# Optimization experiments

Measured on AMD Instinct MI355X. Metric: run time of the kernel, lower is better.

The kernel has to match this reference:

```python
import jax, jax.numpy as jnp
import numpy as np

NUM_EMBEDDINGS = 1024
EMBEDDING_DIM = 64
COMMITMENT_COST = 0.25


def setup_inputs() -> dict:
    key = jax.random.key(0)
    k_in, k_emb = jax.random.split(key)
    inputs = jax.random.normal(k_in, (256, 512, EMBEDDING_DIM), dtype=jnp.float32)
    # nn.init.uniform_(weight, -1/K, 1/K)
    bound = 1.0 / NUM_EMBEDDINGS
    embeddings = jax.random.uniform(
        k_emb, (NUM_EMBEDDINGS, EMBEDDING_DIM), dtype=jnp.float32,
        minval=-bound, maxval=bound)
    return {"inputs": inputs, "embeddings": embeddings}


def reference(inputs, embeddings):
    D = embeddings.shape[1]
    flat = inputs.reshape(-1, D)  # [N, D]
    distances = (
        jnp.sum(flat ** 2, axis=1, keepdims=True)
        - 2.0 * flat @ embeddings.T
        + jnp.sum(embeddings ** 2, axis=1)
    )
    encoding_indices = jnp.argmin(distances, axis=1)  # [N]
    quantized = embeddings[encoding_indices].reshape(inputs.shape)
    e_latent_loss = jnp.mean((jax.lax.stop_gradient(quantized) - inputs) ** 2)
    q_latent_loss = jnp.mean((quantized - jax.lax.stop_gradient(inputs)) ** 2)
    loss = q_latent_loss + COMMITMENT_COST * e_latent_loss
    # straight-through estimator
    quantized = inputs + jax.lax.stop_gradient(quantized - inputs)
    return quantized, loss
```

## Files before the change

### kernel.cpp

```cpp
#include <hip/hip_runtime.h>


typedef __attribute__((ext_vector_type(4))) float f32x4;
typedef __attribute__((ext_vector_type(2))) unsigned long long u64x2;

constexpr int N_ROWS = 256 * 512;
constexpr int D      = 64;
constexpr int K      = 1024;
constexpr int TPB    = 256;
constexpr int ROWS_PER_WAVE  = 16;
constexpr int ROWS_PER_BLOCK = 64;
constexpr int NBLK   = N_ROWS / ROWS_PER_BLOCK;
constexpr int CHUNK  = 128;
constexpr int NCHUNK = K / CHUNK;
constexpr int TPC    = CHUNK / 16;

__global__ __launch_bounds__(64) void vq_prep_kernel(
    const float* __restrict__ emb, uint4* __restrict__ ebf) {
  int k = blockIdx.x * 64 + threadIdx.x;
  if (k >= K) return;
  const float* e = emb + (size_t)k * D;
  const int crow = k & 15;
  uint4* row = ebf + ((size_t)(k >> 4) * 1024 + (size_t)crow * 64) / 16;
  const int sw = (crow >> 1) & 3;
#pragma unroll
  for (int s = 0; s < 4; ++s) {
    float4 a0 = *(const float4*)(e + s * 8);
    float4 a1 = *(const float4*)(e + s * 8 + 4);
    float4 b0 = *(const float4*)(e + 32 + s * 8);
    float4 b1 = *(const float4*)(e + 32 + s * 8 + 4);
    const float sc = -1024.f;
    int d0 = 0, d1 = 0, d2 = 0, d3 = 0;
    d0 = __builtin_amdgcn_cvt_pk_fp8_f32(sc * a0.x, sc * a0.y, d0, false);
    d0 = __builtin_amdgcn_cvt_pk_fp8_f32(sc * a0.z, sc * a0.w, d0, true);
    d1 = __builtin_amdgcn_cvt_pk_fp8_f32(sc * a1.x, sc * a1.y, d1, false);
    d1 = __builtin_amdgcn_cvt_pk_fp8_f32(sc * a1.z, sc * a1.w, d1, true);
    d2 = __builtin_amdgcn_cvt_pk_fp8_f32(sc * b0.x, sc * b0.y, d2, false);
    d2 = __builtin_amdgcn_cvt_pk_fp8_f32(sc * b0.z, sc * b0.w, d2, true);
    d3 = __builtin_amdgcn_cvt_pk_fp8_f32(sc * b1.x, sc * b1.y, d3, false);
    d3 = __builtin_amdgcn_cvt_pk_fp8_f32(sc * b1.z, sc * b1.w, d3, true);
    uint4 slot;
    slot.x = (unsigned)d0; slot.y = (unsigned)d1;
    slot.z = (unsigned)d2; slot.w = (unsigned)d3;
    row[s ^ sw] = slot;
  }
}

__global__ __launch_bounds__(TPB, 6) void vq_main_kernel(
    const float* __restrict__ x, const uint4* __restrict__ ebf,
    const float* __restrict__ emb, float* __restrict__ out,
    float* __restrict__ partial) {
  __shared__ uint4 se[2][CHUNK * 4];
  __shared__ int   s_bi[ROWS_PER_BLOCK];
  __shared__ float s_w[TPB / 64];

  const int tid  = threadIdx.x;
  const int wave = tid >> 6, lane = tid & 63;
  const int lrow = lane & 15;
  const int kseg = lane >> 4;

  uint4 st0[2];
#pragma unroll
  for (int i = 0; i < 2; ++i) st0[i] = ebf[i * 256 + tid];

  const size_t rbase =
      (size_t)blockIdx.x * ROWS_PER_BLOCK + (size_t)wave * ROWS_PER_WAVE;

  long long xa[2];
  {
    const float* p = x + (rbase + lrow) * D + kseg * 8;
#pragma unroll
    for (int h = 0; h < 2; ++h) {
      float4 a = *(const float4*)(p + h * 32);
      float4 b = *(const float4*)(p + h * 32 + 4);
      int d0 = 0, d1 = 0;
      d0 = __builtin_amdgcn_cvt_pk_fp8_f32(a.x, a.y, d0, false);
      d0 = __builtin_amdgcn_cvt_pk_fp8_f32(a.z, a.w, d0, true);
      d1 = __builtin_amdgcn_cvt_pk_fp8_f32(b.x, b.y, d1, false);
      d1 = __builtin_amdgcn_cvt_pk_fp8_f32(b.z, b.w, d1, true);
      xa[h] = (long long)(((unsigned long long)(unsigned)d1 << 32) |
                          (unsigned long long)(unsigned)d0);
    }
  }

#pragma unroll
  for (int i = 0; i < 2; ++i) se[0][i * 256 + tid] = st0[i];

  unsigned kmin[4];
#pragma unroll
  for (int j = 0; j < 4; ++j) kmin[j] = 0xFFFFFFFFu;

  const f32x4 c512 = {512.f, 512.f, 512.f, 512.f};

  __syncthreads();

  const int off = lrow * 64 + ((kseg ^ ((lrow >> 1) & 3)) << 4);

  int cur = 0;
  for (int c = 0; c < NCHUNK; ++c) {
    uint4 stg[2];
    if (c + 1 < NCHUNK) {
#pragma unroll
      for (int i = 0; i < 2; ++i)
        stg[i] = ebf[(c + 1) * 512 + i * 256 + tid];
    }

    const char* base = (const char*)&se[cur][0];
#pragma unroll
    for (int tt = 0; tt < TPC; ++tt) {
      u64x2 ev = *(const u64x2*)(base + (tt << 10) + off);
      const int kcode = c * CHUNK + tt * 16 + lrow;
      f32x4 acc = __builtin_amdgcn_mfma_f32_16x16x32_fp8_fp8(
          xa[0], (long long)ev[0], c512, 0, 0, 0);
      acc = __builtin_amdgcn_mfma_f32_16x16x32_fp8_fp8(
          xa[1], (long long)ev[1], acc, 0, 0, 0);
#pragma unroll
      for (int j = 0; j < 4; ++j) {
        unsigned key = (__builtin_bit_cast(unsigned, acc[j]) & 0xFFFFFC00u) |
                       (unsigned)kcode;
        kmin[j] = kmin[j] < key ? kmin[j] : key;
      }
    }

    if (c + 1 < NCHUNK) {
#pragma unroll
      for (int i = 0; i < 2; ++i) se[cur ^ 1][i * 256 + tid] = stg[i];
    }
    __syncthreads();
    cur ^= 1;
  }

#pragma unroll
  for (int m = 1; m <= 8; m <<= 1) {
#pragma unroll
    for (int j = 0; j < 4; ++j) {
      unsigned o = (unsigned)__shfl_xor((int)kmin[j], m, 64);
      kmin[j] = kmin[j] < o ? kmin[j] : o;
    }
  }

  if (lrow < 4) {
    unsigned v = (lrow == 0) ? kmin[0] : (lrow == 1) ? kmin[1]
               : (lrow == 2) ? kmin[2] : kmin[3];
    s_bi[wave * ROWS_PER_WAVE + kseg * 4 + lrow] = (int)(v & 1023u);
  }

  const int rig = lane >> 4;
  const int chk = lane & 15;
  float lp = 0.f;
#pragma unroll
  for (int g = 0; g < ROWS_PER_WAVE / 4; ++g) {
    const int wrow = g * 4 + rig;
    const size_t r = rbase + wrow;
    const int bi = s_bi[wave * ROWS_PER_WAVE + wrow];
    float4 xv = ((const float4*)(x + r * D))[chk];
    float4 qv = ((const float4*)(emb + (size_t)bi * D))[chk];
    float dx = qv.x - xv.x, dy = qv.y - xv.y;
    float dz = qv.z - xv.z, dw = qv.w - xv.w;
    lp = fmaf(dx, dx, lp); lp = fmaf(dy, dy, lp);
    lp = fmaf(dz, dz, lp); lp = fmaf(dw, dw, lp);
    float4 ov;
    ov.x = xv.x + dx; ov.y = xv.y + dy;
    ov.z = xv.z + dz; ov.w = xv.w + dw;
    ((float4*)(out + r * D))[chk] = ov;
  }

#pragma unroll
  for (int o2 = 32; o2 > 0; o2 >>= 1) lp += __shfl_down(lp, o2, 64);
  if (lane == 0) s_w[wave] = lp;
  __syncthreads();
  if (tid == 0)
    partial[blockIdx.x] = (s_w[0] + s_w[1]) + (s_w[2] + s_w[3]);
}

__global__ __launch_bounds__(256) void vq_loss_kernel(
    const float* __restrict__ partial, float* __restrict__ out) {
  __shared__ float wsum[4];
  int tid = threadIdx.x;
  float v = 0.f;
#pragma unroll
  for (int i = 0; i < NBLK / 256; ++i) v += partial[tid + i * 256];
#pragma unroll
  for (int off = 32; off > 0; off >>= 1) v += __shfl_down(v, off, 64);
  if ((tid & 63) == 0) wsum[tid >> 6] = v;
  __syncthreads();
  if (tid == 0) {
    float total = (wsum[0] + wsum[1]) + (wsum[2] + wsum[3]);
    out[(size_t)N_ROWS * D] = 1.25f * total / (float)((size_t)N_ROWS * D);
  }
}

extern "C" void kernel_launch(void* const* d_in, const int* in_sizes, int n_in,
                              void* d_out, int out_size, void* d_ws,
                              size_t ws_size, hipStream_t stream) {
  const float* x   = (const float*)d_in[0];
  const float* emb = (const float*)d_in[1];
  float* out = (float*)d_out;

  char* ws = (char*)d_ws;
  float* partial = (float*)ws;
  uint4* ebf     = (uint4*)(ws + 8192);

  vq_prep_kernel<<<16, 64, 0, stream>>>(emb, ebf);
  vq_main_kernel<<<NBLK, TPB, 0, stream>>>(x, ebf, emb, out, partial);
  vq_loss_kernel<<<1, 256, 0, stream>>>(partial, out);
}
```

Baseline: 34.46 us.

## Keep codebook quarters in registers per wave, drop LDS chunk pipeline

Each wave now holds a quarter of the fp8 codebook (256 codes) in registers and computes distances for all 64 block rows against it. This replaces the double-buffered LDS streaming of codebook chunks and its per-chunk barriers. Per-wave partial argmin keys are merged through a small shared array. The cost is much higher register pressure: each thread holds 16 uint4 of codebook data plus 16 kmin accumulators, and the occupancy hint drops from 6 to 3.

```diff
diff --git a/kernel.cpp b/kernel.cpp
--- a/kernel.cpp
+++ b/kernel.cpp
@@ -2,27 +2,22 @@
 
 
 typedef __attribute__((ext_vector_type(4))) float f32x4;
-typedef __attribute__((ext_vector_type(2))) unsigned long long u64x2;
 
 constexpr int N_ROWS = 256 * 512;
 constexpr int D      = 64;
 constexpr int K      = 1024;
 constexpr int TPB    = 256;
-constexpr int ROWS_PER_WAVE  = 16;
-constexpr int ROWS_PER_BLOCK = 64;
-constexpr int NBLK   = N_ROWS / ROWS_PER_BLOCK;
-constexpr int CHUNK  = 128;
-constexpr int NCHUNK = K / CHUNK;
-constexpr int TPC    = CHUNK / 16;
+constexpr int RPB    = 64;
+constexpr int NBLK   = N_ROWS / RPB;
+constexpr int KPW    = K / 4;
+constexpr int TPW    = KPW / 16;
 
 __global__ __launch_bounds__(64) void vq_prep_kernel(
     const float* __restrict__ emb, uint4* __restrict__ ebf) {
   int k = blockIdx.x * 64 + threadIdx.x;
   if (k >= K) return;
   const float* e = emb + (size_t)k * D;
-  const int crow = k & 15;
-  uint4* row = ebf + ((size_t)(k >> 4) * 1024 + (size_t)crow * 64) / 16;
-  const int sw = (crow >> 1) & 3;
+  uint4* row = ebf + (size_t)(k >> 4) * 64 + (size_t)(k & 15) * 4;
 #pragma unroll
   for (int s = 0; s < 4; ++s) {
     float4 a0 = *(const float4*)(e + s * 8);
@@ -42,33 +37,33 @@
     uint4 slot;
     slot.x = (unsigned)d0; slot.y = (unsigned)d1;
     slot.z = (unsigned)d2; slot.w = (unsigned)d3;
-    row[s ^ sw] = slot;
+    row[s] = slot;
   }
 }
 
-__global__ __launch_bounds__(TPB, 6) void vq_main_kernel(
+__global__ __launch_bounds__(TPB, 3) void vq_main_kernel(
     const float* __restrict__ x, const uint4* __restrict__ ebf,
     const float* __restrict__ emb, float* __restrict__ out,
     float* __restrict__ partial) {
-  __shared__ uint4 se[2][CHUNK * 4];
-  __shared__ int   s_bi[ROWS_PER_BLOCK];
-  __shared__ float s_w[TPB / 64];
+  __shared__ unsigned s_key[RPB][4];
+  __shared__ float    s_w[4];
 
   const int tid  = threadIdx.x;
   const int wave = tid >> 6, lane = tid & 63;
   const int lrow = lane & 15;
   const int kseg = lane >> 4;
 
-  uint4 st0[2];
+  uint4 xe[TPW];
 #pragma unroll
-  for (int i = 0; i < 2; ++i) st0[i] = ebf[i * 256 + tid];
+  for (int t = 0; t < TPW; ++t)
+    xe[t] = ebf[(wave * TPW + t) * 64 + lrow * 4 + kseg];
 
-  const size_t rbase =
-      (size_t)blockIdx.x * ROWS_PER_BLOCK + (size_t)wave * ROWS_PER_WAVE;
+  const size_t rbase = (size_t)blockIdx.x * RPB;
 
-  long long xa[2];
-  {
-    const float* p = x + (rbase + lrow) * D + kseg * 8;
+  long long xa[4][2];
+#pragma unroll
+  for (int rg = 0; rg < 4; ++rg) {
+    const float* p = x + (rbase + rg * 16 + lrow) * D + kseg * 8;
 #pragma unroll
     for (int h = 0; h < 2; ++h) {
       float4 a = *(const float4*)(p + h * 32);
@@ -78,81 +73,74 @@
       d0 = __builtin_amdgcn_cvt_pk_fp8_f32(a.z, a.w, d0, true);
       d1 = __builtin_amdgcn_cvt_pk_fp8_f32(b.x, b.y, d1, false);
       d1 = __builtin_amdgcn_cvt_pk_fp8_f32(b.z, b.w, d1, true);
-      xa[h] = (long long)(((unsigned long long)(unsigned)d1 << 32) |
-                          (unsigned long long)(unsigned)d0);
+      xa[rg][h] = (long long)(((unsigned long long)(unsigned)d1 << 32) |
+                              (unsigned long long)(unsigned)d0);
     }
   }
 
+  unsigned kmin[4][4];
 #pragma unroll
-  for (int i = 0; i < 2; ++i) se[0][i * 256 + tid] = st0[i];
-
-  unsigned kmin[4];
+  for (int rg = 0; rg < 4; ++rg)
 #pragma unroll
-  for (int j = 0; j < 4; ++j) kmin[j] = 0xFFFFFFFFu;
+    for (int j = 0; j < 4; ++j) kmin[rg][j] = 0xFFFFFFFFu;
 
   const f32x4 c512 = {512.f, 512.f, 512.f, 512.f};
 
-  __syncthreads();
-
-  const int off = lrow * 64 + ((kseg ^ ((lrow >> 1) & 3)) << 4);
-
-  int cur = 0;
-  for (int c = 0; c < NCHUNK; ++c) {
-    uint4 stg[2];
-    if (c + 1 < NCHUNK) {
 #pragma unroll
-      for (int i = 0; i < 2; ++i)
-        stg[i] = ebf[(c + 1) * 512 + i * 256 + tid];
-    }
-
-    const char* base = (const char*)&se[cur][0];
+  for (int t = 0; t < TPW; ++t) {
+    long long ev0 = (long long)(((unsigned long long)xe[t].y << 32) |
+                                (unsigned long long)xe[t].x);
+    long long ev1 = (long long)(((unsigned long long)xe[t].w << 32) |
+                                (unsigned long long)xe[t].z);
+    const unsigned code = (unsigned)(wave * KPW + t * 16 + lrow);
 #pragma unroll
-    for (int tt = 0; tt < TPC; ++tt) {
-      u64x2 ev = *(const u64x2*)(base + (tt << 10) + off);
-      const int kcode = c * CHUNK + tt * 16 + lrow;
+    for (int rg = 0; rg < 4; ++rg) {
       f32x4 acc = __builtin_amdgcn_mfma_f32_16x16x32_fp8_fp8(
-          xa[0], (long long)ev[0], c512, 0, 0, 0);
+          xa[rg][0], ev0, c512, 0, 0, 0);
       acc = __builtin_amdgcn_mfma_f32_16x16x32_fp8_fp8(
-          xa[1], (long long)ev[1], acc, 0, 0, 0);
+          xa[rg][1], ev1, acc, 0, 0, 0);
 #pragma unroll
       for (int j = 0; j < 4; ++j) {
         unsigned key = (__builtin_bit_cast(unsigned, acc[j]) & 0xFFFFFC00u) |
-                       (unsigned)kcode;
-        kmin[j] = kmin[j] < key ? kmin[j] : key;
+                       code;
+        kmin[rg][j] = kmin[rg][j] < key ? kmin[rg][j] : key;
       }
     }
-
-    if (c + 1 < NCHUNK) {
-#pragma unroll
-      for (int i = 0; i < 2; ++i) se[cur ^ 1][i * 256 + tid] = stg[i];
-    }
-    __syncthreads();
-    cur ^= 1;
   }
 
 #pragma unroll
   for (int m = 1; m <= 8; m <<= 1) {
 #pragma unroll
-    for (int j = 0; j < 4; ++j) {
-      unsigned o = (unsigned)__shfl_xor((int)kmin[j], m, 64);
-      kmin[j] = kmin[j] < o ? kmin[j] : o;
-    }
+    for (int rg = 0; rg < 4; ++rg)
+#pragma unroll
+      for (int j = 0; j < 4; ++j) {
+        unsigned o = (unsigned)__shfl_xor((int)kmin[rg][j], m, 64);
+        kmin[rg][j] = kmin[rg][j] < o ? kmin[rg][j] : o;
+      }
   }
 
   if (lrow < 4) {
-    unsigned v = (lrow == 0) ? kmin[0] : (lrow == 1) ? kmin[1]
-               : (lrow == 2) ? kmin[2] : kmin[3];
-    s_bi[wave * ROWS_PER_WAVE + kseg * 4 + lrow] = (int)(v & 1023u);
+#pragma unroll
+    for (int rg = 0; rg < 4; ++rg) {
+      unsigned v = (lrow == 0) ? kmin[rg][0] : (lrow == 1) ? kmin[rg][1]
+                 : (lrow == 2) ? kmin[rg][2] : kmin[rg][3];
+      s_key[rg * 16 + kseg * 4 + lrow][wave] = v;
+    }
   }
+  __syncthreads();
 
   const int rig = lane >> 4;
   const int chk = lane & 15;
   float lp = 0.f;
 #pragma unroll
-  for (int g = 0; g < ROWS_PER_WAVE / 4; ++g) {
-    const int wrow = g * 4 + rig;
+  for (int g = 0; g < 4; ++g) {
+    const int wrow = wave * 16 + g * 4 + rig;
     const size_t r = rbase + wrow;
-    const int bi = s_bi[wave * ROWS_PER_WAVE + wrow];
+    uint4 cand = *(const uint4*)&s_key[wrow][0];
+    unsigned k0 = cand.x < cand.y ? cand.x : cand.y;
+    unsigned k1 = cand.z < cand.w ? cand.z : cand.w;
+    unsigned kk = k0 < k1 ? k0 : k1;
+    const int bi = (int)(kk & 1023u);
     float4 xv = ((const float4*)(x + r * D))[chk];
     float4 qv = ((const float4*)(emb + (size_t)bi * D))[chk];
     float dx = qv.x - xv.x, dy = qv.y - xv.y;
```

Result: slower. 41.18 us (+19.5%).
